# Optimization experiments

Measured on AMD Instinct MI355X. Metric: run time of the kernel, lower is better.

Reference implementation:

```python
import jax, jax.numpy as jnp
import numpy as np

E = 8          # num_experts
K = 2          # top-k experts per token
CAP_RATIO = 1.05


def setup_inputs() -> dict:
    key = jax.random.key(0)
    k0, k1, k2, k3 = jax.random.split(key, 4)
    B, S, D, H = 2, 2048, 512, 2048
    return {
        "x": jax.random.normal(k0, (B, S, D), jnp.float32),
        "gate_w": jax.random.normal(k1, (E, D), jnp.float32) * (1.0 / np.sqrt(D)),
        "fc1_w": jax.random.normal(k2, (E, D, H), jnp.float32) * (1.0 / np.sqrt(D)),
        "fc1_b": jnp.zeros((E, H), jnp.float32),
        "fc2_w": jax.random.normal(k3, (E, H, D), jnp.float32) * (1.0 / np.sqrt(H)),
        "fc2_b": jnp.zeros((E, D), jnp.float32),
    }


def reference(x, gate_w, fc1_w, fc1_b, fc2_w, fc2_b):
    B, S, D = x.shape
    xf = x.reshape(-1, D)               # [T, D]
    T = xf.shape[0]

    # ---- router (eval mode: no noise) ----
    logits = xf @ gate_w.T              # [T, E]
    gates = jax.nn.softmax(logits, axis=-1)
    top_g, top_i = jax.lax.top_k(gates, K)   # [T, K]

    # importance auxiliary loss (std unbiased=False == jnp.std default)
    imp = gates.sum(axis=0)                  # [E]
    imp_loss = (jnp.std(imp) / (imp.mean() + 1e-6)) ** 2

    # ---- capacity-limited dispatch mask ----
    # torch loops slot-major: slot 0 over all tokens in order, then slot 1.
    # position of each (slot, token) entry within its expert's queue:
    buffer_cap = round(K * T * CAP_RATIO / E)
    idx_sm = top_i.T.reshape(-1)                        # [K*T] slot-major
    oh = jax.nn.one_hot(idx_sm, E, dtype=jnp.int32)     # [K*T, E]
    pos = jnp.cumsum(oh, axis=0) - oh                   # earlier same-expert count
    pos_e = jnp.take_along_axis(pos, idx_sm[:, None], axis=1)[:, 0]
    within = (pos_e < buffer_cap).reshape(K, T).T       # [T, K] bool

    wf = within.astype(xf.dtype)
    oh_tke = jax.nn.one_hot(top_i, E, dtype=xf.dtype) * wf[..., None]  # dispatch mask [T,K,E]
    combine_te = jnp.einsum('tk,tke->te', top_g * wf, oh_tke / jnp.maximum(oh_tke, 1e-30) * oh_tke) if False else jnp.einsum('tk,tke->te', top_g * wf, jax.nn.one_hot(top_i, E, dtype=xf.dtype))

    # load-balance loss from post-capacity token counts
    tokens_per_expert = oh_tke.sum(axis=(0, 1))         # [E]
    l_load = (jnp.std(tokens_per_expert) / (tokens_per_expert.mean() + 1e-6)) ** 2
    l_aux = 0.5 * (imp_loss + l_load)

    # ---- per-expert MLP (dense compute, masked combine) ----
    h = jnp.einsum('td,edh->teh', xf, fc1_w) + fc1_b[None]      # [T, E, H]
    h = jax.nn.gelu(h, approximate=False)                       # torch nn.GELU default
    y = jnp.einsum('teh,ehd->ted', h, fc2_w) + fc2_b[None]      # [T, E, D]

    out = jnp.einsum('te,ted->td', combine_te, y).reshape(B, S, D)
    return out, l_aux, l_load
```

## Files before the change

### kernel.cpp

```cpp
#include <hip/hip_runtime.h>
#include <hip/hip_bf16.h>

#define E_    8
#define TT    4096
#define DD    512
#define HH    2048
#define CAP   1075
#define MPAD  1152
#define MT    9
#define MT2   18

typedef __bf16 bf16_t;
typedef bf16_t bf16x4 __attribute__((ext_vector_type(4)));
typedef bf16_t bf16x8 __attribute__((ext_vector_type(8)));
typedef float  f32x4  __attribute__((ext_vector_type(4)));
typedef unsigned int u32;

__device__ __forceinline__ bf16_t tobf(float f) { return (bf16_t)f; }

__device__ __forceinline__ float gelu_f(float v) {
  const float u = v * (0.7978845608028654f + 0.035677408136300125f * v * v);
  const float a = __builtin_fabsf(u);
  const float ex = __expf(2.0f * a);
  float th = 1.0f - 2.0f / (ex + 1.0f);
  th = __builtin_copysignf(th, u);
  return 0.5f * v * (1.0f + th);
}

template <int N> __device__ __forceinline__ void waitcnt_vm() {
  static_assert(N == 0 || N == 4 || N == 6, "unsupported vmcnt");
  if constexpr (N == 0) asm volatile("s_waitcnt vmcnt(0)" ::: "memory");
  else if constexpr (N == 4) asm volatile("s_waitcnt vmcnt(4)" ::: "memory");
  else if constexpr (N == 6) asm volatile("s_waitcnt vmcnt(6)" ::: "memory");
}
__device__ __forceinline__ void block_barrier() {
  asm volatile("" ::: "memory");
  __builtin_amdgcn_s_barrier();
  asm volatile("" ::: "memory");
}

#define OFF_ETOK  256u
#define OFF_TOPI  (OFF_ETOK + 8u*1152u*4u)
#define OFF_TOPG  (OFF_TOPI + 4096u*2u*4u)
#define OFF_SLOT  (OFF_TOPG + 4096u*2u*4u)
#define OFF_XB    (OFF_SLOT + 4096u*2u*4u)
#define XB_BYTES  (4096u*512u*2u)
#define OFF_W1T   (OFF_XB + XB_BYTES)
#define W1T_BYTES (8u*512u*2048u*2u)
#define OFF_W2T   (OFF_W1T + W1T_BYTES)
#define W2T_BYTES (8u*2048u*512u*2u)
#define OFF_H     (OFF_W2T + W2T_BYTES)
#define H_BYTES   (8u*1152u*2048u*2u)
#define OFF_Y     OFF_W1T

__global__ __launch_bounds__(256) void router_kernel(
    const float* __restrict__ x, const float* __restrict__ gw,
    float* __restrict__ imp, int* __restrict__ top_i, float* __restrict__ top_g,
    bf16_t* __restrict__ xb) {
  const int tid = threadIdx.x;
  const int wid = tid >> 6, lane = tid & 63;
  const int t = blockIdx.x * 4 + wid;

  float p[E_];
#pragma unroll
  for (int e = 0; e < E_; ++e) p[e] = 0.f;
  const float* xr = x + (size_t)t * DD;
  bf16_t* xo = xb + (size_t)t * DD;
#pragma unroll
  for (int it = 0; it < 2; ++it) {
    const int d = it * 256 + lane * 4;
    const float4 xv = *(const float4*)(xr + d);
    bf16_t o4[4] = {tobf(xv.x), tobf(xv.y), tobf(xv.z), tobf(xv.w)};
    *(bf16x4*)(xo + d) = *(const bf16x4*)o4;
#pragma unroll
    for (int e = 0; e < E_; ++e) {
      const float4 gv = *(const float4*)(gw + e * DD + d);
      p[e] += xv.x * gv.x + xv.y * gv.y + xv.z * gv.z + xv.w * gv.w;
    }
  }
#pragma unroll
  for (int off = 32; off > 0; off >>= 1) {
#pragma unroll
    for (int e = 0; e < E_; ++e) p[e] += __shfl_down(p[e], off);
  }

  __shared__ float simp[4][E_];
  if (lane == 0) {
    float mx = p[0];
#pragma unroll
    for (int e = 1; e < E_; ++e) mx = fmaxf(mx, p[e]);
    float g[E_]; float s = 0.f;
#pragma unroll
    for (int e = 0; e < E_; ++e) { g[e] = expf(p[e] - mx); s += g[e]; }
    const float inv = 1.f / s;
#pragma unroll
    for (int e = 0; e < E_; ++e) { g[e] *= inv; simp[wid][e] = g[e]; }
    int i0 = 0;
#pragma unroll
    for (int e = 1; e < E_; ++e) if (g[e] > g[i0]) i0 = e;
    int i1 = (i0 == 0) ? 1 : 0;
#pragma unroll
    for (int e = 0; e < E_; ++e) if (e != i0 && g[e] > g[i1]) i1 = e;
    top_i[t * 2 + 0] = i0;  top_i[t * 2 + 1] = i1;
    top_g[t * 2 + 0] = g[i0]; top_g[t * 2 + 1] = g[i1];
  }
  __syncthreads();
  if (tid < E_) {
    const float s = simp[0][tid] + simp[1][tid] + simp[2][tid] + simp[3][tid];
    atomicAdd(&imp[tid], s);
  }
}

__global__ __launch_bounds__(1024) void capacity_kernel(
    const int* __restrict__ top_i, const float* __restrict__ top_g,
    const float* __restrict__ imp, int* __restrict__ etok,
    int* __restrict__ slot_map, int* __restrict__ kept, float* __restrict__ scal) {
  __shared__ u32 wt[16][4];
  const int tid = threadIdx.x, wave = tid >> 6, lane = tid & 63;

  int eidx[8];
#pragma unroll
  for (int q = 0; q < 8; ++q) {
    const int j = tid * 8 + q;
    const int k = j >> 12, t = j & (TT - 1);
    eidx[q] = top_i[t * 2 + k];
  }
  u32 pk[4] = {0u, 0u, 0u, 0u};
#pragma unroll
  for (int q = 0; q < 8; ++q) pk[eidx[q] >> 1] += 1u << ((eidx[q] & 1) * 16);

  u32 v[4] = {pk[0], pk[1], pk[2], pk[3]};
#pragma unroll
  for (int off = 1; off < 64; off <<= 1) {
#pragma unroll
    for (int p = 0; p < 4; ++p) {
      const u32 n = (u32)__shfl_up((int)v[p], off);
      if (lane >= off) v[p] += n;
    }
  }
  if (lane == 63) {
#pragma unroll
    for (int p = 0; p < 4; ++p) wt[wave][p] = v[p];
  }
  __syncthreads();
  u32 base[4] = {0u, 0u, 0u, 0u}, tot[4] = {0u, 0u, 0u, 0u};
#pragma unroll
  for (int w = 0; w < 16; ++w) {
#pragma unroll
    for (int p = 0; p < 4; ++p) {
      const u32 xv = wt[w][p];
      if (w < wave) base[p] += xv;
      tot[p] += xv;
    }
  }
  int run[E_];
#pragma unroll
  for (int p = 0; p < 4; ++p) {
    const u32 excl = base[p] + v[p] - pk[p];
    run[2 * p]     = (int)(excl & 0xFFFFu);
    run[2 * p + 1] = (int)(excl >> 16);
  }
#pragma unroll
  for (int q = 0; q < 8; ++q) {
    const int e = eidx[q];
    const int pos = run[e]++;
    const int j = tid * 8 + q;
    if (pos < CAP) {
      const int k = j >> 12, t = j & (TT - 1);
      etok[e * MPAD + pos] = t;
      slot_map[j] = (e << 16) | pos;
    } else {
      slot_map[j] = -1;
    }
  }
  if (tid == 0) {
    float tpe[E_];
#pragma unroll
    for (int p = 0; p < 4; ++p) {
      const int t0 = (int)(tot[p] & 0xFFFFu), t1 = (int)(tot[p] >> 16);
      const int k0 = t0 < CAP ? t0 : CAP, k1 = t1 < CAP ? t1 : CAP;
      kept[2 * p] = k0; kept[2 * p + 1] = k1;
      tpe[2 * p] = (float)k0; tpe[2 * p + 1] = (float)k1;
    }
    float ms = 0.f;
#pragma unroll
    for (int e = 0; e < E_; ++e) ms += tpe[e];
    ms *= (1.f / E_);
    float vt = 0.f;
#pragma unroll
    for (int e = 0; e < E_; ++e) { const float d = tpe[e] - ms; vt += d * d; }
    vt *= (1.f / E_);
    const float ll = vt / ((ms + 1e-6f) * (ms + 1e-6f));

    float iv[E_], mi = 0.f;
#pragma unroll
    for (int e = 0; e < E_; ++e) { iv[e] = imp[e]; mi += iv[e]; }
    mi *= (1.f / E_);
    float vi = 0.f;
#pragma unroll
    for (int e = 0; e < E_; ++e) { const float d = iv[e] - mi; vi += d * d; }
    vi *= (1.f / E_);
    const float il = vi / ((mi + 1e-6f) * (mi + 1e-6f));

    scal[0] = 0.5f * (il + ll);
    scal[1] = ll;
  }
}

__global__ __launch_bounds__(256) void transpose_both_kernel(
    const float* __restrict__ fc1, bf16_t* __restrict__ w1t,
    const float* __restrict__ fc2, bf16_t* __restrict__ w2t) {
  __shared__ float tile[64][65];
  const int z = blockIdx.z;
  const bool first = (z < 8);
  const int e = first ? z : z - 8;
  const int R = first ? DD : HH;
  const int C = first ? HH : DD;
  const int ct = first ? blockIdx.x : blockIdx.y;
  const int rt = first ? blockIdx.y : blockIdx.x;
  const float* ip = (first ? fc1 : fc2) + (size_t)e * DD * HH;
  bf16_t* op = (first ? w1t : w2t) + (size_t)e * DD * HH;
  const int r0 = rt * 64, c0 = ct * 64;
  const int tid = threadIdx.x;
  const int rr = tid >> 4, c4 = (tid & 15) * 4;
#pragma unroll
  for (int p = 0; p < 4; ++p) {
    const int r = p * 16 + rr;
    const float4 v = *(const float4*)(ip + (size_t)(r0 + r) * C + c0 + c4);
    tile[r][c4 + 0] = v.x; tile[r][c4 + 1] = v.y;
    tile[r][c4 + 2] = v.z; tile[r][c4 + 3] = v.w;
  }
  __syncthreads();
  const int g = tid & 7, ob = tid >> 3;
#pragma unroll
  for (int p = 0; p < 2; ++p) {
    const int oc = p * 32 + ob;
    bf16_t o8[8];
#pragma unroll
    for (int k = 0; k < 8; ++k) o8[k] = tobf(tile[g * 8 + k][oc]);
    *(bf16x8*)(op + (size_t)(c0 + oc) * R + r0 + g * 8) = *(const bf16x8*)o8;
  }
}

template <int NW, int MR, int NC, int MI, int KLEN, int KSTR, bool GATHER>
__device__ __forceinline__ void gemm_core(
    const bf16_t* __restrict__ Abase, const int* __restrict__ rows,
    const bf16_t* __restrict__ B,
    bf16_t* As, bf16_t* Bs, f32x4 (&acc)[4][MI]) {
  constexpr int NWC = NC / 64;
  constexpr int AIW = MR / (8 * NW);
  constexpr int BIW = NC / (8 * NW);
  constexpr int L   = AIW + BIW;
  constexpr int NS  = KLEN / 64;
  constexpr int ABUF = MR * 64;
  constexpr int BBUF = NC * 64;
  static_assert(NS >= 2, "need >=2 K-steps");
  const int tid = threadIdx.x;
  const int wave = tid >> 6, lane = tid & 63;
  const int r8 = lane >> 3;
  const int kswz = ((lane & 7) ^ r8) * 8;
  const bf16_t* ga[AIW];
#pragma unroll
  for (int p = 0; p < AIW; ++p) {
    const int r = (wave * AIW + p) * 8 + r8;
    const int trow = GATHER ? rows[r] : r;
    ga[p] = Abase + (size_t)trow * KSTR + kswz;
  }
  const bf16_t* gb = B + (size_t)(wave * BIW * 8 + r8) * KSTR + kswz;
  const int mw = (wave / NWC) * (MI * 16), nw = (wave % NWC) * 64;
  const int l15 = lane & 15, quad = lane >> 4;
  const int sw = l15 & 7;

  auto stage = [&](int s) {
    const int k0 = s * 64;
    bf16_t* as = As + (s & 1) * ABUF;
    bf16_t* bs = Bs + (s & 1) * BBUF;
#pragma unroll
    for (int p = 0; p < AIW; ++p)
      __builtin_amdgcn_global_load_lds(
          (const __attribute__((address_space(1))) void*)(ga[p] + k0),
          (__attribute__((address_space(3))) void*)(as + ((wave * AIW + p) * 8) * 64),
          16, 0, 0);
#pragma unroll
    for (int p = 0; p < BIW; ++p)
      __builtin_amdgcn_global_load_lds(
          (const __attribute__((address_space(1))) void*)(gb + (size_t)p * 8 * KSTR + k0),
          (__attribute__((address_space(3))) void*)(bs + ((wave * BIW + p) * 8) * 64),
          16, 0, 0);
  };
  auto compute = [&](int s) {
    const bf16_t* as = As + (s & 1) * ABUF;
    const bf16_t* bs = Bs + (s & 1) * BBUF;
#pragma unroll
    for (int kh = 0; kh < 2; ++kh) {
      const int kc = ((kh * 4 + quad) ^ sw) << 3;
      bf16x8 af[MI], bfr[4];
#pragma unroll
      for (int i = 0; i < MI; ++i)
        af[i] = *(const bf16x8*)(as + (mw + i * 16 + l15) * 64 + kc);
#pragma unroll
      for (int j = 0; j < 4; ++j)
        bfr[j] = *(const bf16x8*)(bs + (nw + j * 16 + l15) * 64 + kc);
#pragma unroll
      for (int j = 0; j < 4; ++j)
#pragma unroll
        for (int i = 0; i < MI; ++i)
          acc[j][i] = __builtin_amdgcn_mfma_f32_16x16x32_bf16(bfr[j], af[i], acc[j][i], 0, 0, 0);
    }
  };

  stage(0);
  stage(1);
  waitcnt_vm<L>();
  block_barrier();

#pragma unroll
  for (int s = 0; s < NS; ++s) {
    compute(s);
    block_barrier();
    if (s + 2 < NS) {
      stage(s + 2);
      waitcnt_vm<L>();
      block_barrier();
    } else if (s + 1 < NS) {
      waitcnt_vm<0>();
      block_barrier();
    }
  }
}

__global__ __launch_bounds__(512, 4) void gemm1_kernel(
    const bf16_t* __restrict__ xb, const int* __restrict__ etok,
    const int* __restrict__ kept, const bf16_t* __restrict__ W1t,
    const float* __restrict__ b1, bf16_t* __restrict__ Hbuf) {
  const int e = blockIdx.x, tileN = blockIdx.y, tileM = blockIdx.z;
  if (tileM * 128 >= kept[e]) return;
  __shared__ __align__(16) bf16_t As[2 * 128 * 64];
  __shared__ __align__(16) bf16_t Bs[2 * 128 * 64];
  const bf16_t* B = W1t + ((size_t)e * HH + tileN * 128) * DD;
  f32x4 acc[4][2];
  const f32x4 z = {0.f, 0.f, 0.f, 0.f};
#pragma unroll
  for (int j = 0; j < 4; ++j)
#pragma unroll
    for (int i = 0; i < 2; ++i) acc[j][i] = z;
  gemm_core<8, 128, 128, 2, DD, DD, true>(xb, etok + e * MPAD + tileM * 128, B, As, Bs, acc);

  const int tid = threadIdx.x, wave = tid >> 6, lane = tid & 63;
  const int mw = (wave >> 1) * 32, nw = (wave & 1) * 64;
  const int l15 = lane & 15, quad = lane >> 4;
#pragma unroll
  for (int j = 0; j < 4; ++j) {
    const int n0 = tileN * 128 + nw + j * 16 + quad * 4;
    const float4 b4 = *(const float4*)(b1 + e * HH + n0);
#pragma unroll
    for (int i = 0; i < 2; ++i) {
      const int m = tileM * 128 + mw + i * 16 + l15;
      bf16x4 h4;
      h4.x = tobf(gelu_f(acc[j][i][0] + b4.x));
      h4.y = tobf(gelu_f(acc[j][i][1] + b4.y));
      h4.z = tobf(gelu_f(acc[j][i][2] + b4.z));
      h4.w = tobf(gelu_f(acc[j][i][3] + b4.w));
      *(bf16x4*)(Hbuf + ((size_t)e * MPAD + m) * HH + n0) = h4;
    }
  }
}

__global__ __launch_bounds__(256, 4) void gemm2_kernel(
    const bf16_t* __restrict__ Hbuf, const bf16_t* __restrict__ W2t,
    const int* __restrict__ kept, bf16_t* __restrict__ Ybuf) {
  const int e = blockIdx.x, tileN = blockIdx.y, tileM = blockIdx.z;
  const int nk = kept[e];
  if (tileM * 64 >= nk) return;
  __shared__ __align__(16) bf16_t As[2 * 64 * 64];
  __shared__ __align__(16) bf16_t Bs[2 * 128 * 64];
  const bf16_t* A = Hbuf + ((size_t)e * MPAD + tileM * 64) * HH;
  const bf16_t* B = W2t + ((size_t)e * DD + tileN * 128) * HH;
  f32x4 acc[4][2];
  const f32x4 z = {0.f, 0.f, 0.f, 0.f};
#pragma unroll
  for (int j = 0; j < 4; ++j)
#pragma unroll
    for (int i = 0; i < 2; ++i) acc[j][i] = z;
  gemm_core<4, 64, 128, 2, HH, HH, false>(A, nullptr, B, As, Bs, acc);

  const int tid = threadIdx.x, wave = tid >> 6, lane = tid & 63;
  const int mw = (wave >> 1) * 32, nw = (wave & 1) * 64;
  const int l15 = lane & 15, quad = lane >> 4;
#pragma unroll
  for (int j = 0; j < 4; ++j) {
    const int n0 = tileN * 128 + nw + j * 16 + quad * 4;
#pragma unroll
    for (int i = 0; i < 2; ++i) {
      const int m = tileM * 64 + mw + i * 16 + l15;
      if (m < nk) {
        bf16x4 o4;
        o4.x = tobf(acc[j][i][0]);
        o4.y = tobf(acc[j][i][1]);
        o4.z = tobf(acc[j][i][2]);
        o4.w = tobf(acc[j][i][3]);
        *(bf16x4*)(Ybuf + ((size_t)e * MPAD + m) * DD + n0) = o4;
      }
    }
  }
}

__global__ __launch_bounds__(128) void combine_kernel(
    const bf16_t* __restrict__ Ybuf, const float* __restrict__ b2,
    const int* __restrict__ slot_map, const float* __restrict__ top_g,
    float* __restrict__ out) {
  const int t = blockIdx.x;
  const int c = threadIdx.x * 4;
  float4 acc = {0.f, 0.f, 0.f, 0.f};
#pragma unroll
  for (int k = 0; k < 2; ++k) {
    const int sm = slot_map[k * TT + t];
    if (sm >= 0) {
      const int e = sm >> 16, pos = sm & 0xFFFF;
      const float w = top_g[t * 2 + k];
      const bf16x4 y4 = *(const bf16x4*)(Ybuf + ((size_t)e * MPAD + pos) * DD + c);
      const float4 bb = *(const float4*)(b2 + e * DD + c);
      acc.x += w * ((float)y4.x + bb.x);
      acc.y += w * ((float)y4.y + bb.y);
      acc.z += w * ((float)y4.z + bb.z);
      acc.w += w * ((float)y4.w + bb.w);
    }
  }
  *(float4*)(out + (size_t)t * DD + c) = acc;
}

extern "C" void kernel_launch(void* const* d_in, const int* in_sizes, int n_in,
                              void* d_out, int out_size, void* d_ws, size_t ws_size,
                              hipStream_t stream) {
  const float* x      = (const float*)d_in[0];
  const float* gate_w = (const float*)d_in[1];
  const float* fc1_w  = (const float*)d_in[2];
  const float* fc1_b  = (const float*)d_in[3];
  const float* fc2_w  = (const float*)d_in[4];
  const float* fc2_b  = (const float*)d_in[5];
  float* out = (float*)d_out;

  char* ws = (char*)d_ws;
  float*  imp   = (float*)(ws + 0);
  int*    kept  = (int*)(ws + 64);
  int*    etok  = (int*)(ws + OFF_ETOK);
  int*    top_i = (int*)(ws + OFF_TOPI);
  float*  top_g = (float*)(ws + OFF_TOPG);
  int*    slotm = (int*)(ws + OFF_SLOT);
  bf16_t* xb    = (bf16_t*)(ws + OFF_XB);
  bf16_t* W1t   = (bf16_t*)(ws + OFF_W1T);
  bf16_t* W2t   = (bf16_t*)(ws + OFF_W2T);
  bf16_t* Hbuf  = (bf16_t*)(ws + OFF_H);
  bf16_t* Ybuf  = (bf16_t*)(ws + OFF_Y);
  float*  scal  = out + (size_t)TT * DD;

  hipMemsetAsync(ws, 0, OFF_TOPI, stream);

  transpose_both_kernel<<<dim3(32, 8, 16), 256, 0, stream>>>(fc1_w, W1t, fc2_w, W2t);

  router_kernel<<<TT / 4, 256, 0, stream>>>(x, gate_w, imp, top_i, top_g, xb);
  capacity_kernel<<<1, 1024, 0, stream>>>(top_i, top_g, imp, etok, slotm, kept, scal);

  gemm1_kernel<<<dim3(E_, HH / 128, MT), 512, 0, stream>>>(xb, etok, kept, W1t, fc1_b, Hbuf);
  gemm2_kernel<<<dim3(E_, DD / 128, MT2), 256, 0, stream>>>(Hbuf, W2t, kept, Ybuf);
  combine_kernel<<<TT, 128, 0, stream>>>(Ybuf, fc2_b, slotm, top_g, out);
}
```

Before: 212.5 us.

## Switch expert GEMMs to 32x32x16 MFMA with 64x64 wave tiles

Replaces the 16x16x32 bf16 MFMA inner loop with 32x32x16 MFMAs. Each wave now owns a 64x64 output tile, so block sizes halve: 256 threads for gemm1 and 128 for gemm2. The aim is to cut LDS fragment reads per MFMA and to issue fewer, larger matrix instructions, raising reuse per wave. In exchange there are fewer waves per block to hide latency, more global loads per wave (hence the higher vmcnt thresholds), and a new epilogue layout mapping.

```diff
diff --git a/kernel.cpp b/kernel.cpp
--- a/kernel.cpp
+++ b/kernel.cpp
@@ -8,12 +8,12 @@
 #define CAP   1075
 #define MPAD  1152
 #define MT    9
-#define MT2   18
 
 typedef __bf16 bf16_t;
 typedef bf16_t bf16x4 __attribute__((ext_vector_type(4)));
 typedef bf16_t bf16x8 __attribute__((ext_vector_type(8)));
 typedef float  f32x4  __attribute__((ext_vector_type(4)));
+typedef float  f32x16 __attribute__((ext_vector_type(16)));
 typedef unsigned int u32;
 
 __device__ __forceinline__ bf16_t tobf(float f) { return (bf16_t)f; }
@@ -28,10 +28,10 @@
 }
 
 template <int N> __device__ __forceinline__ void waitcnt_vm() {
-  static_assert(N == 0 || N == 4 || N == 6, "unsupported vmcnt");
+  static_assert(N == 0 || N == 8 || N == 12, "unsupported vmcnt");
   if constexpr (N == 0) asm volatile("s_waitcnt vmcnt(0)" ::: "memory");
-  else if constexpr (N == 4) asm volatile("s_waitcnt vmcnt(4)" ::: "memory");
-  else if constexpr (N == 6) asm volatile("s_waitcnt vmcnt(6)" ::: "memory");
+  else if constexpr (N == 8) asm volatile("s_waitcnt vmcnt(8)" ::: "memory");
+  else if constexpr (N == 12) asm volatile("s_waitcnt vmcnt(12)" ::: "memory");
 }
 __device__ __forceinline__ void block_barrier() {
   asm volatile("" ::: "memory");
@@ -242,11 +242,11 @@
   }
 }
 
-template <int NW, int MR, int NC, int MI, int KLEN, int KSTR, bool GATHER>
+template <int NW, int MR, int NC, int KLEN, int KSTR, bool GATHER>
 __device__ __forceinline__ void gemm_core(
     const bf16_t* __restrict__ Abase, const int* __restrict__ rows,
     const bf16_t* __restrict__ B,
-    bf16_t* As, bf16_t* Bs, f32x4 (&acc)[4][MI]) {
+    bf16_t* As, bf16_t* Bs, f32x16 (&acc)[2][2]) {
   constexpr int NWC = NC / 64;
   constexpr int AIW = MR / (8 * NW);
   constexpr int BIW = NC / (8 * NW);
@@ -255,6 +255,7 @@
   constexpr int ABUF = MR * 64;
   constexpr int BBUF = NC * 64;
   static_assert(NS >= 2, "need >=2 K-steps");
+  static_assert(MR == (NW / NWC) * 64, "wave grid must tile MR");
   const int tid = threadIdx.x;
   const int wave = tid >> 6, lane = tid & 63;
   const int r8 = lane >> 3;
@@ -267,9 +268,8 @@
     ga[p] = Abase + (size_t)trow * KSTR + kswz;
   }
   const bf16_t* gb = B + (size_t)(wave * BIW * 8 + r8) * KSTR + kswz;
-  const int mw = (wave / NWC) * (MI * 16), nw = (wave % NWC) * 64;
-  const int l15 = lane & 15, quad = lane >> 4;
-  const int sw = l15 & 7;
+  const int mw = (wave / NWC) * 64, nw = (wave % NWC) * 64;
+  const int l31 = lane & 31, khi = lane >> 5, l7 = lane & 7;
 
   auto stage = [&](int s) {
     const int k0 = s * 64;
@@ -292,20 +292,20 @@
     const bf16_t* as = As + (s & 1) * ABUF;
     const bf16_t* bs = Bs + (s & 1) * BBUF;
 #pragma unroll
-    for (int kh = 0; kh < 2; ++kh) {
-      const int kc = ((kh * 4 + quad) ^ sw) << 3;
-      bf16x8 af[MI], bfr[4];
-#pragma unroll
-      for (int i = 0; i < MI; ++i)
-        af[i] = *(const bf16x8*)(as + (mw + i * 16 + l15) * 64 + kc);
-#pragma unroll
-      for (int j = 0; j < 4; ++j)
-        bfr[j] = *(const bf16x8*)(bs + (nw + j * 16 + l15) * 64 + kc);
-#pragma unroll
-      for (int j = 0; j < 4; ++j)
-#pragma unroll
-        for (int i = 0; i < MI; ++i)
-          acc[j][i] = __builtin_amdgcn_mfma_f32_16x16x32_bf16(bfr[j], af[i], acc[j][i], 0, 0, 0);
+    for (int ks = 0; ks < 4; ++ks) {
+      const int ch = (((ks * 2 + khi) ^ l7) << 3);
+      bf16x8 af[2], bfr[2];
+#pragma unroll
+      for (int i = 0; i < 2; ++i)
+        af[i] = *(const bf16x8*)(as + (mw + i * 32 + l31) * 64 + ch);
+#pragma unroll
+      for (int j = 0; j < 2; ++j)
+        bfr[j] = *(const bf16x8*)(bs + (nw + j * 32 + l31) * 64 + ch);
+#pragma unroll
+      for (int j = 0; j < 2; ++j)
+#pragma unroll
+        for (int i = 0; i < 2; ++i)
+          acc[j][i] = __builtin_amdgcn_mfma_f32_32x32x16_bf16(bfr[j], af[i], acc[j][i], 0, 0, 0);
     }
   };
 
@@ -329,7 +329,7 @@
   }
 }
 
-__global__ __launch_bounds__(512, 4) void gemm1_kernel(
+__global__ __launch_bounds__(256, 4) void gemm1_kernel(
     const bf16_t* __restrict__ xb, const int* __restrict__ etok,
     const int* __restrict__ kept, const bf16_t* __restrict__ W1t,
     const float* __restrict__ b1, bf16_t* __restrict__ Hbuf) {
@@ -338,35 +338,38 @@
   __shared__ __align__(16) bf16_t As[2 * 128 * 64];
   __shared__ __align__(16) bf16_t Bs[2 * 128 * 64];
   const bf16_t* B = W1t + ((size_t)e * HH + tileN * 128) * DD;
-  f32x4 acc[4][2];
-  const f32x4 z = {0.f, 0.f, 0.f, 0.f};
-#pragma unroll
-  for (int j = 0; j < 4; ++j)
-#pragma unroll
-    for (int i = 0; i < 2; ++i) acc[j][i] = z;
-  gemm_core<8, 128, 128, 2, DD, DD, true>(xb, etok + e * MPAD + tileM * 128, B, As, Bs, acc);
+  f32x16 acc[2][2];
+#pragma unroll
+  for (int j = 0; j < 2; ++j)
+#pragma unroll
+    for (int i = 0; i < 2; ++i)
+#pragma unroll
+      for (int r = 0; r < 16; ++r) acc[j][i][r] = 0.f;
+  gemm_core<4, 128, 128, DD, DD, true>(xb, etok + e * MPAD + tileM * 128, B, As, Bs, acc);
 
   const int tid = threadIdx.x, wave = tid >> 6, lane = tid & 63;
-  const int mw = (wave >> 1) * 32, nw = (wave & 1) * 64;
-  const int l15 = lane & 15, quad = lane >> 4;
-#pragma unroll
-  for (int j = 0; j < 4; ++j) {
-    const int n0 = tileN * 128 + nw + j * 16 + quad * 4;
-    const float4 b4 = *(const float4*)(b1 + e * HH + n0);
-#pragma unroll
-    for (int i = 0; i < 2; ++i) {
-      const int m = tileM * 128 + mw + i * 16 + l15;
-      bf16x4 h4;
-      h4.x = tobf(gelu_f(acc[j][i][0] + b4.x));
-      h4.y = tobf(gelu_f(acc[j][i][1] + b4.y));
-      h4.z = tobf(gelu_f(acc[j][i][2] + b4.z));
-      h4.w = tobf(gelu_f(acc[j][i][3] + b4.w));
-      *(bf16x4*)(Hbuf + ((size_t)e * MPAD + m) * HH + n0) = h4;
-    }
-  }
-}
-
-__global__ __launch_bounds__(256, 4) void gemm2_kernel(
+  const int mw = (wave >> 1) * 64, nw = (wave & 1) * 64;
+  const int l31 = lane & 31, khi = lane >> 5;
+#pragma unroll
+  for (int j = 0; j < 2; ++j)
+#pragma unroll
+    for (int r2 = 0; r2 < 4; ++r2) {
+      const int n0 = tileN * 128 + nw + j * 32 + r2 * 8 + khi * 4;
+      const float4 b4 = *(const float4*)(b1 + e * HH + n0);
+#pragma unroll
+      for (int i = 0; i < 2; ++i) {
+        const int m = tileM * 128 + mw + i * 32 + l31;
+        bf16x4 h4;
+        h4.x = tobf(gelu_f(acc[j][i][r2 * 4 + 0] + b4.x));
+        h4.y = tobf(gelu_f(acc[j][i][r2 * 4 + 1] + b4.y));
+        h4.z = tobf(gelu_f(acc[j][i][r2 * 4 + 2] + b4.z));
+        h4.w = tobf(gelu_f(acc[j][i][r2 * 4 + 3] + b4.w));
+        *(bf16x4*)(Hbuf + ((size_t)e * MPAD + m) * HH + n0) = h4;
+      }
+    }
+}
+
+__global__ __launch_bounds__(128, 4) void gemm2_kernel(
     const bf16_t* __restrict__ Hbuf, const bf16_t* __restrict__ W2t,
     const int* __restrict__ kept, bf16_t* __restrict__ Ybuf) {
   const int e = blockIdx.x, tileN = blockIdx.y, tileM = blockIdx.z;
@@ -376,33 +379,36 @@
   __shared__ __align__(16) bf16_t Bs[2 * 128 * 64];
   const bf16_t* A = Hbuf + ((size_t)e * MPAD + tileM * 64) * HH;
   const bf16_t* B = W2t + ((size_t)e * DD + tileN * 128) * HH;
-  f32x4 acc[4][2];
-  const f32x4 z = {0.f, 0.f, 0.f, 0.f};
-#pragma unroll
-  for (int j = 0; j < 4; ++j)
-#pragma unroll
-    for (int i = 0; i < 2; ++i) acc[j][i] = z;
-  gemm_core<4, 64, 128, 2, HH, HH, false>(A, nullptr, B, As, Bs, acc);
+  f32x16 acc[2][2];
+#pragma unroll
+  for (int j = 0; j < 2; ++j)
+#pragma unroll
+    for (int i = 0; i < 2; ++i)
+#pragma unroll
+      for (int r = 0; r < 16; ++r) acc[j][i][r] = 0.f;
+  gemm_core<2, 64, 128, HH, HH, false>(A, nullptr, B, As, Bs, acc);
 
   const int tid = threadIdx.x, wave = tid >> 6, lane = tid & 63;
-  const int mw = (wave >> 1) * 32, nw = (wave & 1) * 64;
-  const int l15 = lane & 15, quad = lane >> 4;
-#pragma unroll
-  for (int j = 0; j < 4; ++j) {
-    const int n0 = tileN * 128 + nw + j * 16 + quad * 4;
-#pragma unroll
-    for (int i = 0; i < 2; ++i) {
-      const int m = tileM * 64 + mw + i * 16 + l15;
-      if (m < nk) {
-        bf16x4 o4;
-        o4.x = tobf(acc[j][i][0]);
-        o4.y = tobf(acc[j][i][1]);
-        o4.z = tobf(acc[j][i][2]);
-        o4.w = tobf(acc[j][i][3]);
-        *(bf16x4*)(Ybuf + ((size_t)e * MPAD + m) * DD + n0) = o4;
+  const int nw = wave * 64;
+  const int l31 = lane & 31, khi = lane >> 5;
+#pragma unroll
+  for (int j = 0; j < 2; ++j)
+#pragma unroll
+    for (int r2 = 0; r2 < 4; ++r2) {
+      const int n0 = tileN * 128 + nw + j * 32 + r2 * 8 + khi * 4;
+#pragma unroll
+      for (int i = 0; i < 2; ++i) {
+        const int m = tileM * 64 + i * 32 + l31;
+        if (m < nk) {
+          bf16x4 o4;
+          o4.x = tobf(acc[j][i][r2 * 4 + 0]);
+          o4.y = tobf(acc[j][i][r2 * 4 + 1]);
+          o4.z = tobf(acc[j][i][r2 * 4 + 2]);
+          o4.w = tobf(acc[j][i][r2 * 4 + 3]);
+          *(bf16x4*)(Ybuf + ((size_t)e * MPAD + m) * DD + n0) = o4;
+        }
       }
     }
-  }
 }
 
 __global__ __launch_bounds__(128) void combine_kernel(
@@ -461,7 +467,7 @@
   router_kernel<<<TT / 4, 256, 0, stream>>>(x, gate_w, imp, top_i, top_g, xb);
   capacity_kernel<<<1, 1024, 0, stream>>>(top_i, top_g, imp, etok, slotm, kept, scal);
 
-  gemm1_kernel<<<dim3(E_, HH / 128, MT), 512, 0, stream>>>(xb, etok, kept, W1t, fc1_b, Hbuf);
-  gemm2_kernel<<<dim3(E_, DD / 128, MT2), 256, 0, stream>>>(Hbuf, W2t, kept, Ybuf);
+  gemm1_kernel<<<dim3(E_, HH / 128, MT), 256, 0, stream>>>(xb, etok, kept, W1t, fc1_b, Hbuf);
+  gemm2_kernel<<<dim3(E_, DD / 128, MT * 2), 128, 0, stream>>>(Hbuf, W2t, kept, Ybuf);
   combine_kernel<<<TT, 128, 0, stream>>>(Ybuf, fc2_b, slotm, top_g, out);
 }
```

New measurement: 220.9 us. 4.0% more time.
